# Kernel tuning notes

Measured on AMD Instinct MI355X. Metric: run time of the kernel, lower is better.

The kernel has to match this reference:

```python
import jax, jax.numpy as jnp
import numpy as np

H = 16
EMB = 1024
DH = 64  # att_dim


def setup_inputs() -> dict:
    key = jax.random.key(0)
    k1, k2, k3 = jax.random.split(key, 3)
    B, T = 4, 2048
    x = jax.random.normal(k1, (B, T, EMB), dtype=jnp.float32)
    # torch nn.Linear weight layout: [out_features, in_features]
    w_qkv = jax.random.normal(k2, (3 * H * DH, EMB), dtype=jnp.float32) * (1.0 / np.sqrt(EMB))
    wo = jax.random.normal(k3, (EMB, H * DH), dtype=jnp.float32) * (1.0 / np.sqrt(H * DH))
    return {"x": x, "w_qkv": w_qkv, "wo": wo}


def reference(x, w_qkv, wo):
    B, T, C = x.shape
    qkv = jnp.einsum('btc,oc->bto', x, w_qkv)  # [B,T,3*H*DH]
    q, k, v = jnp.split(qkv, 3, axis=-1)
    # [B,H,T,DH]
    q = q.reshape(B, T, H, DH).transpose(0, 2, 1, 3)
    k = k.reshape(B, T, H, DH).transpose(0, 2, 1, 3)
    v = v.reshape(B, T, H, DH).transpose(0, 2, 1, 3)
    scale = 1.0 / np.sqrt(DH).astype(np.float32)
    scores = jnp.einsum('bhqd,bhkd->bhqk', q, k) * scale
    causal = jnp.tril(jnp.ones((T, T), dtype=bool))
    scores = jnp.where(causal, scores, jnp.finfo(scores.dtype).min)
    attn = jax.nn.softmax(scores, axis=-1)
    y = jnp.einsum('bhqk,bhkd->bhqd', attn, v)  # [B,H,T,DH]
    y = y.transpose(0, 2, 1, 3).reshape(B, T, H * DH)
    return jnp.einsum('bti,oi->bto', y, wo)
```

## Files before the change

### kernel.cpp

```cpp
#include <hip/hip_runtime.h>
#include <hip/hip_bf16.h>
#include <stdint.h>


typedef __attribute__((ext_vector_type(8))) short short8;
typedef __attribute__((ext_vector_type(4))) float floatx4;

extern "C" __device__ float __ocml_native_exp2_f32(float);

__device__ __forceinline__ ushort f2bf(float f) {
  uint32_t u = __float_as_uint(f);
  u += 0x7fff + ((u >> 16) & 1);
  return (ushort)(u >> 16);
}

#if __has_builtin(__builtin_amdgcn_cvt_pk_bf16_f32)
typedef __attribute__((ext_vector_type(2))) __bf16 bf16x2;
__device__ __forceinline__ uint32_t pack_bf16(float a, float b) {
  union { bf16x2 v; uint32_t u; } cv;
  cv.v = __builtin_amdgcn_cvt_pk_bf16_f32(a, b);
  return cv.u;
}
#else
__device__ __forceinline__ uint32_t pack_bf16(float a, float b) {
  uint32_t ua = __float_as_uint(a) + 0x8000u;
  uint32_t ub = __float_as_uint(b) + 0x8000u;
  return __builtin_amdgcn_perm(ub, ua, 0x07060302u);
}
#endif

__device__ __forceinline__ void gload16(const ushort* g, ushort* l) {
  __builtin_amdgcn_global_load_lds(
      (const __attribute__((address_space(1))) void*)g,
      (__attribute__((address_space(3))) void*)l, 16, 0, 0);
}

__global__ __launch_bounds__(256) void cvt3_kernel(const float* __restrict__ x,
                                                   const float* __restrict__ wq,
                                                   const float* __restrict__ wo,
                                                   ushort* __restrict__ xo,
                                                   ushort* __restrict__ wqo,
                                                   ushort* __restrict__ woo) {
  int i = blockIdx.x * 256 + threadIdx.x;
  const float* in; ushort* out; int idx;
  if (i < 2097152)      { in = x;  out = xo;  idx = i; }
  else if (i < 2883584) { in = wq; out = wqo; idx = i - 2097152; }
  else                  { in = wo; out = woo; idx = i - 2883584; }
  float4 v = ((const float4*)in)[idx];
  ushort4 o;
  o.x = f2bf(v.x); o.y = f2bf(v.y); o.z = f2bf(v.z); o.w = f2bf(v.w);
  ((ushort4*)out)[idx] = o;
}

__global__ __launch_bounds__(512) void gemm256(const ushort* __restrict__ A,
                                               const ushort* __restrict__ Bw,
                                               ushort* __restrict__ qb,
                                               ushort* __restrict__ kb,
                                               ushort* __restrict__ vt) {
  constexpr int SLOT = 12288;
  __shared__ ushort ring[3 * SLOT];
  int tid = threadIdx.x;
  int lane = tid & 63, wave = tid >> 6;
  int lrow = lane & 15, quad = lane >> 4;
  int wm = wave >> 1, wn = wave & 1;
  int wm64 = wm * 64, wn64 = wn * 64;
  int m0 = blockIdx.x * 256, n0 = blockIdx.y * 128;

  int srow = tid >> 2;
  int schunk8 = ((tid & 3) ^ ((tid >> 3) & 3)) * 8;
  const ushort* Ag0 = A + (size_t)(m0 + srow) * 1024 + schunk8;
  const ushort* Ag1 = Ag0 + (size_t)128 * 1024;
  const ushort* Bg0 = Bw + (size_t)(n0 + srow) * 1024 + schunk8;
  int fo2 = (quad ^ ((lrow >> 1) & 3)) * 8;

  const floatx4 zero4 = {0.f, 0.f, 0.f, 0.f};
  floatx4 acc[4][4];
#pragma unroll
  for (int i = 0; i < 4; i++)
#pragma unroll
    for (int j = 0; j < 4; j++) acc[i][j] = zero4;

  auto stage = [&](int t) {
    ushort* Sa = &ring[(t % 3) * SLOT];
    size_t kk = (size_t)t * 32;
    gload16(Ag0 + kk, &Sa[wave * 16 * 32]);
    gload16(Ag1 + kk, &Sa[(128 + wave * 16) * 32]);
    gload16(Bg0 + kk, &Sa[8192 + wave * 16 * 32]);
  };

  short8 fAa[4], fAb[4], fBa[4], fBb[4];

#define READF(u_, FN)                                                         \
  {                                                                           \
    ushort* As_ = &ring[((u_) % 3) * SLOT];                                   \
    ushort* Bs_ = As_ + 8192;                                                 \
    _Pragma("unroll")                                                         \
    for (int mi = 0; mi < 4; mi++)                                            \
      FN##a[mi] = *(const short8*)(&As_[(wm64 + mi * 16 + lrow) * 32 + fo2]); \
    _Pragma("unroll")                                                         \
    for (int nj = 0; nj < 4; nj++)                                            \
      FN##b[nj] = *(const short8*)(&Bs_[(wn64 + nj * 16 + lrow) * 32 + fo2]); \
  }

#define MFMAS(FC)                                                             \
  {                                                                           \
    __builtin_amdgcn_s_setprio(1);                                            \
    _Pragma("unroll")                                                         \
    for (int mi = 0; mi < 4; mi++)                                            \
      _Pragma("unroll")                                                       \
      for (int nj = 0; nj < 4; nj++)                                          \
        acc[mi][nj] = __builtin_amdgcn_mfma_f32_16x16x32_bf16(                \
            FC##a[mi], FC##b[nj], acc[mi][nj], 0, 0, 0);                      \
    __builtin_amdgcn_s_setprio(0);                                            \
  }

#define BARRIER(N_)                                                           \
  asm volatile("s_waitcnt vmcnt(" #N_ ")" ::: "memory");                      \
  __builtin_amdgcn_s_barrier();                                               \
  asm volatile("" ::: "memory");

#define KITER(u_, N_, ISSUE_, FC, FN)                                         \
  {                                                                           \
    BARRIER(N_)                                                               \
    READF(u_, FN)                                                             \
    if (ISSUE_) stage((u_) + 2);                                              \
    MFMAS(FC)                                                                 \
  }

  stage(0); stage(1);
  BARRIER(3)
  READF(0, fA)
  stage(2);
#pragma unroll 1
  for (int p = 0; p < 14; ++p) {
    KITER(2 * p + 1, 3, true, fA, fB);
    KITER(2 * p + 2, 3, true, fB, fA);
  }
  KITER(29, 3, true, fA, fB);
  KITER(30, 3, false, fB, fA);
  KITER(31, 0, false, fA, fB);
  MFMAS(fB)

#undef KITER
#undef BARRIER
#undef MFMAS
#undef READF

  constexpr int CS = 136;
  ushort* sm = ring;
  int sec = n0 >> 10;
  int hrow = tid >> 4, kcol = tid & 15;
  __syncthreads();

  if (sec < 2) {
    float qs = (sec == 0) ? 0.18033688f : 1.0f;
    ushort* dst = (sec == 0) ? qb : kb;
    int hbase = n0 & 1023;
#pragma unroll 1
    for (int hf = 0; hf < 2; ++hf) {
      if ((wm >> 1) == hf) {
#pragma unroll
        for (int mi = 0; mi < 4; mi++)
#pragma unroll
          for (int nj = 0; nj < 4; nj++)
#pragma unroll
            for (int r = 0; r < 4; r++)
              sm[((wm & 1) * 64 + mi * 16 + quad * 4 + r) * CS +
                 wn64 + nj * 16 + lrow] = f2bf(acc[mi][nj][r] * qs);
      }
      __syncthreads();
#pragma unroll
      for (int mi = 0; mi < 4; mi++) {
        int mloc = mi * 32 + hrow;
        int m = m0 + hf * 128 + mloc, b_ = m >> 11, t = m & 2047;
        int col = kcol * 8;
        int h = (hbase + col) >> 6, d = col & 63;
        uint4 val = *(const uint4*)(&sm[mloc * CS + col]);
        *(uint4*)(dst + ((size_t)(b_ * 16 + h) * 2048 + t) * 64 + d) = val;
      }
      __syncthreads();
    }
  } else {
    int b_ = m0 >> 11, t0 = m0 & 2047;
#pragma unroll 1
    for (int hf = 0; hf < 2; ++hf) {
      if ((wm >> 1) == hf) {
#pragma unroll
        for (int mi = 0; mi < 4; mi++)
#pragma unroll
          for (int nj = 0; nj < 4; nj++) {
            uint2 w;
            w.x = pack_bf16(acc[mi][nj][0], acc[mi][nj][1]);
            w.y = pack_bf16(acc[mi][nj][2], acc[mi][nj][3]);
            *(uint2*)(&sm[(wn64 + nj * 16 + lrow) * CS +
                          (wm & 1) * 64 + mi * 16 + quad * 4]) = w;
          }
      }
      __syncthreads();
#pragma unroll
      for (int di = 0; di < 4; di++) {
        int nloc = di * 32 + hrow;
        int n = n0 + nloc, h = (n & 1023) >> 6, d = n & 63;
        uint4 val = *(const uint4*)(&sm[nloc * CS + kcol * 8]);
        *(uint4*)(vt + ((size_t)(b_ * 16 + h) * 64 + d) * 2048 +
                  t0 + hf * 128 + kcol * 8) = val;
      }
      __syncthreads();
    }
  }
}

__global__ __launch_bounds__(256) void gemm_out(const ushort* __restrict__ A,
                                                const ushort* __restrict__ Bw,
                                                float* __restrict__ Cf) {
  constexpr int SLOT = 8192;
  __shared__ ushort ring[3 * SLOT];
  int tid = threadIdx.x;
  int lane = tid & 63, wave = tid >> 6;
  int lrow = lane & 15, quad = lane >> 4;
  int wr = (wave >> 1) * 64, wc = (wave & 1) * 64;
  int m0 = blockIdx.x * 128, n0 = blockIdx.y * 128;

  int srow = tid >> 2;
  int schunk8 = ((tid & 3) ^ ((tid >> 3) & 3)) * 8;
  const ushort* Ag0 = A + (size_t)(m0 + srow) * 1024 + schunk8;
  const ushort* Ag1 = Ag0 + (size_t)64 * 1024;
  const ushort* Bg0 = Bw + (size_t)(n0 + srow) * 1024 + schunk8;
  const ushort* Bg1 = Bg0 + (size_t)64 * 1024;
  int fo2 = (quad ^ ((lrow >> 1) & 3)) * 8;

  const floatx4 zero4 = {0.f, 0.f, 0.f, 0.f};
  floatx4 acc[4][4];
#pragma unroll
  for (int i = 0; i < 4; i++)
#pragma unroll
    for (int j = 0; j < 4; j++) acc[i][j] = zero4;

  auto stage = [&](int t) {
    ushort* Sa = &ring[(t % 3) * SLOT];
    size_t kk = (size_t)t * 32;
    gload16(Ag0 + kk, &Sa[wave * 16 * 32]);
    gload16(Ag1 + kk, &Sa[(64 + wave * 16) * 32]);
    gload16(Bg0 + kk, &Sa[4096 + wave * 16 * 32]);
    gload16(Bg1 + kk, &Sa[4096 + (64 + wave * 16) * 32]);
  };

  short8 fAa[4], fAb[4], fBa[4], fBb[4];

#define READF(u_, FN)                                                         \
  {                                                                           \
    ushort* As_ = &ring[((u_) % 3) * SLOT];                                   \
    ushort* Bs_ = As_ + 4096;                                                 \
    _Pragma("unroll")                                                         \
    for (int mi = 0; mi < 4; mi++)                                            \
      FN##a[mi] = *(const short8*)(&As_[(wr + mi * 16 + lrow) * 32 + fo2]);   \
    _Pragma("unroll")                                                         \
    for (int nj = 0; nj < 4; nj++)                                            \
      FN##b[nj] = *(const short8*)(&Bs_[(wc + nj * 16 + lrow) * 32 + fo2]);   \
  }

#define MFMAS(FC)                                                             \
  {                                                                           \
    __builtin_amdgcn_s_setprio(1);                                            \
    _Pragma("unroll")                                                         \
    for (int mi = 0; mi < 4; mi++)                                            \
      _Pragma("unroll")                                                       \
      for (int nj = 0; nj < 4; nj++)                                          \
        acc[mi][nj] = __builtin_amdgcn_mfma_f32_16x16x32_bf16(                \
            FC##a[mi], FC##b[nj], acc[mi][nj], 0, 0, 0);                      \
    __builtin_amdgcn_s_setprio(0);                                            \
  }

#define BARRIER(N_)                                                           \
  asm volatile("s_waitcnt vmcnt(" #N_ ")" ::: "memory");                      \
  __builtin_amdgcn_s_barrier();                                               \
  asm volatile("" ::: "memory");

#define KITER(u_, N_, ISSUE_, FC, FN)                                         \
  {                                                                           \
    BARRIER(N_)                                                               \
    READF(u_, FN)                                                             \
    if (ISSUE_) stage((u_) + 2);                                              \
    MFMAS(FC)                                                                 \
  }

  stage(0); stage(1);
  BARRIER(4)
  READF(0, fA)
  stage(2);
#pragma unroll 1
  for (int p = 0; p < 14; ++p) {
    KITER(2 * p + 1, 4, true, fA, fB);
    KITER(2 * p + 2, 4, true, fB, fA);
  }
  KITER(29, 4, true, fA, fB);
  KITER(30, 4, false, fB, fA);
  KITER(31, 0, false, fA, fB);
  MFMAS(fB)

#undef KITER
#undef BARRIER
#undef MFMAS
#undef READF

#pragma unroll
  for (int mi = 0; mi < 4; mi++)
#pragma unroll
    for (int nj = 0; nj < 4; nj++)
#pragma unroll
      for (int r = 0; r < 4; r++) {
        int m = m0 + wr + mi * 16 + quad * 4 + r;
        int n = n0 + wc + nj * 16 + lrow;
        Cf[(size_t)m * 1024 + n] = acc[mi][nj][r];
      }
}

__global__ __launch_bounds__(512) void attn_kernel(const ushort* __restrict__ qg,
                                                   const ushort* __restrict__ kg,
                                                   const ushort* __restrict__ vg,
                                                   ushort* __restrict__ y) {
  __shared__ ushort Ks[64 * 64];
  __shared__ ushort Vs[64 * 64];
  __shared__ ushort Ps[8 * 16 * 72];
  int tid = threadIdx.x;
  int lane = tid & 63, wave = tid >> 6;
  int lrow = lane & 15, quad = lane >> 4;
  int gx = blockIdx.x, gy = blockIdx.y;
  int pr = gy >> 3;
  int bh = (gy & 7) * 8 + gx;
  const ushort* qp = qg + (size_t)bh * 2048 * 64;
  const ushort* kp = kg + (size_t)bh * 2048 * 64;
  const ushort* vp = vg + (size_t)bh * 64 * 2048;
  int b = bh >> 4, h = bh & 15;
  int srow = tid >> 3, sc = tid & 7;
  int sswz = ((sc ^ (srow & 7)) * 8);
  int fo = (quad ^ (lrow & 7)) * 8;
  ushort* Pw = &Ps[wave * 16 * 72];

  const floatx4 zero4 = {0.f, 0.f, 0.f, 0.f};
  short8 ones;
#pragma unroll
  for (int i = 0; i < 8; i++) ones[i] = (short)0x3F80;

#pragma unroll 1
  for (int pass = 0; pass < 2; ++pass) {
    int qt = pass ? (15 - pr) : pr;
    int last = 2 * qt + 1;

    const ushort* qrow_p = qp + (size_t)((qt << 7) + wave * 16 + lrow) * 64;
    short8 a_q0 = *(const short8*)(qrow_p + quad * 8);
    short8 a_q1 = *(const short8*)(qrow_p + (quad ^ 4) * 8);

    uint4 kreg = *(const uint4*)(kp + (size_t)srow * 64 + sc * 8);
    uint4 vreg = *(const uint4*)(vp + (size_t)srow * 2048 + sc * 8);

    floatx4 l_acc = zero4;
    floatx4 o_acc[4];
#pragma unroll
    for (int j = 0; j < 4; j++) o_acc[j] = zero4;

#pragma unroll 1
    for (int kv = 0; kv <= last; kv++) {
      asm volatile("" ::: "memory");
      __builtin_amdgcn_s_barrier();
      asm volatile("" ::: "memory");
      *(uint4*)(&Ks[srow * 64 + sswz]) = kreg;
      *(uint4*)(&Vs[srow * 64 + sswz]) = vreg;
      if (kv < last) {
        kreg = *(const uint4*)(kp + (size_t)((kv + 1) * 64 + srow) * 64 + sc * 8);
        vreg = *(const uint4*)(vp + (size_t)srow * 2048 + (kv + 1) * 64 + sc * 8);
      }
      asm volatile("s_waitcnt lgkmcnt(0)" ::: "memory");
      __builtin_amdgcn_s_barrier();
      asm volatile("" ::: "memory");

      floatx4 s[4];
#pragma unroll
      for (int ct = 0; ct < 4; ct++) {
        short8 k0 = *(const short8*)(&Ks[(ct * 16 + lrow) * 64 + fo]);
        short8 k1 = *(const short8*)(&Ks[(ct * 16 + lrow) * 64 + (fo ^ 32)]);
        floatx4 z = zero4;
        z = __builtin_amdgcn_mfma_f32_16x16x32_bf16(k0, a_q0, z, 0, 0, 0);
        z = __builtin_amdgcn_mfma_f32_16x16x32_bf16(k1, a_q1, z, 0, 0, 0);
        s[ct] = z;
      }

      if (kv >= 2 * qt) {
        int qabs = (qt << 7) + wave * 16 + lrow;
        int kbase = (kv << 6) + quad * 4;
#pragma unroll
        for (int ct = 0; ct < 4; ct++)
#pragma unroll
          for (int r = 0; r < 4; r++)
            if (kbase + ct * 16 + r > qabs) s[ct][r] = -1e30f;
      }

#pragma unroll
      for (int ct = 0; ct < 4; ct++) {
        float p0 = __ocml_native_exp2_f32(s[ct][0]);
        float p1 = __ocml_native_exp2_f32(s[ct][1]);
        float p2 = __ocml_native_exp2_f32(s[ct][2]);
        float p3 = __ocml_native_exp2_f32(s[ct][3]);
        uint2 w;
        w.x = pack_bf16(p0, p1);
        w.y = pack_bf16(p2, p3);
        *(uint2*)(&Pw[lrow * 72 + ct * 16 + quad * 4]) = w;
      }
      asm volatile("" ::: "memory");

      short8 a_p0 = *(const short8*)(&Pw[lrow * 72 + quad * 8]);
      short8 a_p1 = *(const short8*)(&Pw[lrow * 72 + 32 + quad * 8]);
      l_acc = __builtin_amdgcn_mfma_f32_16x16x32_bf16(a_p0, ones, l_acc, 0, 0, 0);
      l_acc = __builtin_amdgcn_mfma_f32_16x16x32_bf16(a_p1, ones, l_acc, 0, 0, 0);
#pragma unroll
      for (int j = 0; j < 4; j++) {
        short8 v0 = *(const short8*)(&Vs[(j * 16 + lrow) * 64 + fo]);
        short8 v1 = *(const short8*)(&Vs[(j * 16 + lrow) * 64 + (fo ^ 32)]);
        o_acc[j] = __builtin_amdgcn_mfma_f32_16x16x32_bf16(a_p0, v0, o_acc[j], 0, 0, 0);
        o_acc[j] = __builtin_amdgcn_mfma_f32_16x16x32_bf16(a_p1, v1, o_acc[j], 0, 0, 0);
      }
    }

    float inv[4];
#pragma unroll
    for (int r = 0; r < 4; r++) inv[r] = 1.0f / l_acc[r];

#pragma unroll
    for (int j = 0; j < 4; j++)
#pragma unroll
      for (int r = 0; r < 4; r++) {
        int t = (qt << 7) + wave * 16 + quad * 4 + r;
        y[((size_t)b * 2048 + t) * 1024 + h * 64 + j * 16 + lrow] =
            f2bf(o_acc[j][r] * inv[r]);
      }
  }
}

extern "C" void kernel_launch(void* const* d_in, const int* in_sizes, int n_in,
                              void* d_out, int out_size, void* d_ws, size_t ws_size,
                              hipStream_t stream) {
  const float* x     = (const float*)d_in[0];
  const float* w_qkv = (const float*)d_in[1];
  const float* wo    = (const float*)d_in[2];
  float* out = (float*)d_out;

  ushort* x_bf    = (ushort*)d_ws;
  ushort* wqkv_bf = x_bf + (size_t)8192 * 1024;
  ushort* wo_bf   = wqkv_bf + (size_t)3072 * 1024;
  ushort* qb      = wo_bf + (size_t)1024 * 1024;
  ushort* kb      = qb + (size_t)8388608;
  ushort* vt      = kb + (size_t)8388608;
  ushort* yb      = x_bf;

  cvt3_kernel<<<12288, 256, 0, stream>>>(x, w_qkv, wo, x_bf, wqkv_bf, wo_bf);
  gemm256<<<dim3(32, 24), 512, 0, stream>>>(x_bf, wqkv_bf, qb, kb, vt);
  attn_kernel<<<dim3(8, 64), 512, 0, stream>>>(qb, kb, vt, yb);
  gemm_out<<<dim3(64, 8), 256, 0, stream>>>(yb, wo_bf, out);
}
```

Measured before the change: 218.7 us.

## Enlarge QKV GEMM tile to 256x256 with 8-wide per-wave M fragments

Grows the QKV projection GEMM block tile from 256x128 to 256x256, with waves arranged 2x4 and each wave computing 128x64 (32 accumulators). The aim is more operand reuse per loaded byte and half as many blocks, 384 instead of 768. The register double-buffering of fragments is replaced by a single fragment load per iteration with rotating slot indices, and the epilogue is rewritten for the wider tile. The cost is higher register pressure and shared memory (96KB ring), lower occupancy, and a 384-block grid that may fill the CUs unevenly.

Result: slower. 227.0 us (+3.8%).

```diff
diff --git a/kernel.cpp b/kernel.cpp
--- a/kernel.cpp
+++ b/kernel.cpp
@@ -57,154 +57,148 @@
                                                ushort* __restrict__ qb,
                                                ushort* __restrict__ kb,
                                                ushort* __restrict__ vt) {
-  constexpr int SLOT = 12288;
+  constexpr int SLOT = 16384;
   __shared__ ushort ring[3 * SLOT];
   int tid = threadIdx.x;
   int lane = tid & 63, wave = tid >> 6;
   int lrow = lane & 15, quad = lane >> 4;
-  int wm = wave >> 1, wn = wave & 1;
-  int wm64 = wm * 64, wn64 = wn * 64;
-  int m0 = blockIdx.x * 256, n0 = blockIdx.y * 128;
+  int wm = wave >> 2, wn = wave & 3;
+  int wm128 = wm * 128, wn64 = wn * 64;
+  int m0 = blockIdx.x * 256, n0 = blockIdx.y * 256;
 
   int srow = tid >> 2;
   int schunk8 = ((tid & 3) ^ ((tid >> 3) & 3)) * 8;
   const ushort* Ag0 = A + (size_t)(m0 + srow) * 1024 + schunk8;
   const ushort* Ag1 = Ag0 + (size_t)128 * 1024;
   const ushort* Bg0 = Bw + (size_t)(n0 + srow) * 1024 + schunk8;
+  const ushort* Bg1 = Bg0 + (size_t)128 * 1024;
   int fo2 = (quad ^ ((lrow >> 1) & 3)) * 8;
 
   const floatx4 zero4 = {0.f, 0.f, 0.f, 0.f};
-  floatx4 acc[4][4];
-#pragma unroll
-  for (int i = 0; i < 4; i++)
+  floatx4 acc[8][4];
+#pragma unroll
+  for (int i = 0; i < 8; i++)
 #pragma unroll
     for (int j = 0; j < 4; j++) acc[i][j] = zero4;
 
-  auto stage = [&](int t) {
-    ushort* Sa = &ring[(t % 3) * SLOT];
+  auto stage = [&](int slot, int t) {
+    ushort* Sa = &ring[slot * SLOT];
     size_t kk = (size_t)t * 32;
-    gload16(Ag0 + kk, &Sa[wave * 16 * 32]);
-    gload16(Ag1 + kk, &Sa[(128 + wave * 16) * 32]);
-    gload16(Bg0 + kk, &Sa[8192 + wave * 16 * 32]);
+    gload16(Ag0 + kk, &Sa[wave * 512]);
+    gload16(Ag1 + kk, &Sa[4096 + wave * 512]);
+    gload16(Bg0 + kk, &Sa[8192 + wave * 512]);
+    gload16(Bg1 + kk, &Sa[12288 + wave * 512]);
   };
-
-  short8 fAa[4], fAb[4], fBa[4], fBb[4];
-
-#define READF(u_, FN)                                                         \
-  {                                                                           \
-    ushort* As_ = &ring[((u_) % 3) * SLOT];                                   \
-    ushort* Bs_ = As_ + 8192;                                                 \
-    _Pragma("unroll")                                                         \
-    for (int mi = 0; mi < 4; mi++)                                            \
-      FN##a[mi] = *(const short8*)(&As_[(wm64 + mi * 16 + lrow) * 32 + fo2]); \
-    _Pragma("unroll")                                                         \
-    for (int nj = 0; nj < 4; nj++)                                            \
-      FN##b[nj] = *(const short8*)(&Bs_[(wn64 + nj * 16 + lrow) * 32 + fo2]); \
-  }
-
-#define MFMAS(FC)                                                             \
-  {                                                                           \
-    __builtin_amdgcn_s_setprio(1);                                            \
-    _Pragma("unroll")                                                         \
-    for (int mi = 0; mi < 4; mi++)                                            \
-      _Pragma("unroll")                                                       \
-      for (int nj = 0; nj < 4; nj++)                                          \
-        acc[mi][nj] = __builtin_amdgcn_mfma_f32_16x16x32_bf16(                \
-            FC##a[mi], FC##b[nj], acc[mi][nj], 0, 0, 0);                      \
-    __builtin_amdgcn_s_setprio(0);                                            \
-  }
 
 #define BARRIER(N_)                                                           \
   asm volatile("s_waitcnt vmcnt(" #N_ ")" ::: "memory");                      \
   __builtin_amdgcn_s_barrier();                                               \
   asm volatile("" ::: "memory");
 
-#define KITER(u_, N_, ISSUE_, FC, FN)                                         \
+#define COMPUTE(CUR_, DOSTAGE_, NXT_, T_)                                     \
   {                                                                           \
-    BARRIER(N_)                                                               \
-    READF(u_, FN)                                                             \
-    if (ISSUE_) stage((u_) + 2);                                              \
-    MFMAS(FC)                                                                 \
-  }
-
-  stage(0); stage(1);
-  BARRIER(3)
-  READF(0, fA)
-  stage(2);
-#pragma unroll 1
-  for (int p = 0; p < 14; ++p) {
-    KITER(2 * p + 1, 3, true, fA, fB);
-    KITER(2 * p + 2, 3, true, fB, fA);
-  }
-  KITER(29, 3, true, fA, fB);
-  KITER(30, 3, false, fB, fA);
-  KITER(31, 0, false, fA, fB);
-  MFMAS(fB)
-
-#undef KITER
+    ushort* As_ = &ring[(CUR_)*SLOT];                                         \
+    ushort* Bs_ = As_ + 8192;                                                 \
+    short8 a_[8], b_[4];                                                      \
+    _Pragma("unroll")                                                         \
+    for (int mi = 0; mi < 8; mi++)                                            \
+      a_[mi] = *(const short8*)(&As_[(wm128 + mi * 16 + lrow) * 32 + fo2]);   \
+    _Pragma("unroll")                                                         \
+    for (int nj = 0; nj < 4; nj++)                                            \
+      b_[nj] = *(const short8*)(&Bs_[(wn64 + nj * 16 + lrow) * 32 + fo2]);    \
+    if (DOSTAGE_) stage((NXT_), (T_));                                        \
+    __builtin_amdgcn_s_setprio(1);                                            \
+    _Pragma("unroll")                                                         \
+    for (int mi = 0; mi < 8; mi++)                                            \
+      _Pragma("unroll")                                                       \
+      for (int nj = 0; nj < 4; nj++)                                          \
+        acc[mi][nj] = __builtin_amdgcn_mfma_f32_16x16x32_bf16(                \
+            a_[mi], b_[nj], acc[mi][nj], 0, 0, 0);                            \
+    __builtin_amdgcn_s_setprio(0);                                            \
+  }
+
+  stage(0, 0); stage(1, 1);
+  int cur = 0, nxt = 2;
+#pragma unroll 1
+  for (int u = 0; u < 30; ++u) {
+    BARRIER(4)
+    COMPUTE(cur, true, nxt, u + 2)
+    cur = (cur == 2) ? 0 : cur + 1;
+    nxt = (nxt == 2) ? 0 : nxt + 1;
+  }
+  BARRIER(4)
+  COMPUTE(cur, false, 0, 0)
+  cur = (cur == 2) ? 0 : cur + 1;
+  BARRIER(0)
+  COMPUTE(cur, false, 0, 0)
+
+#undef COMPUTE
 #undef BARRIER
-#undef MFMAS
-#undef READF
-
-  constexpr int CS = 136;
+
+  constexpr int CS = 264;
   ushort* sm = ring;
   int sec = n0 >> 10;
-  int hrow = tid >> 4, kcol = tid & 15;
+  int b_ = m0 >> 11, t0 = m0 & 2047;
+  int hb = (n0 & 1023) >> 6;
   __syncthreads();
 
   if (sec < 2) {
     float qs = (sec == 0) ? 0.18033688f : 1.0f;
     ushort* dst = (sec == 0) ? qb : kb;
-    int hbase = n0 & 1023;
+    int kcol = tid & 7, hrow = tid >> 3;
 #pragma unroll 1
     for (int hf = 0; hf < 2; ++hf) {
-      if ((wm >> 1) == hf) {
-#pragma unroll
-        for (int mi = 0; mi < 4; mi++)
+      if (wm == hf) {
+#pragma unroll
+        for (int mi = 0; mi < 8; mi++)
 #pragma unroll
           for (int nj = 0; nj < 4; nj++)
 #pragma unroll
             for (int r = 0; r < 4; r++)
-              sm[((wm & 1) * 64 + mi * 16 + quad * 4 + r) * CS +
-                 wn64 + nj * 16 + lrow] = f2bf(acc[mi][nj][r] * qs);
+              sm[(mi * 16 + quad * 4 + r) * CS + wn64 + nj * 16 + lrow] =
+                  f2bf(acc[mi][nj][r] * qs);
       }
       __syncthreads();
 #pragma unroll
-      for (int mi = 0; mi < 4; mi++) {
-        int mloc = mi * 32 + hrow;
-        int m = m0 + hf * 128 + mloc, b_ = m >> 11, t = m & 2047;
-        int col = kcol * 8;
-        int h = (hbase + col) >> 6, d = col & 63;
-        uint4 val = *(const uint4*)(&sm[mloc * CS + col]);
-        *(uint4*)(dst + ((size_t)(b_ * 16 + h) * 2048 + t) * 64 + d) = val;
-      }
+      for (int ri = 0; ri < 2; ri++)
+#pragma unroll
+        for (int hh = 0; hh < 4; hh++) {
+          int mloc = ri * 64 + hrow;
+          uint4 val = *(const uint4*)(&sm[mloc * CS + hh * 64 + kcol * 8]);
+          int t = t0 + hf * 128 + mloc;
+          *(uint4*)(dst + ((size_t)(b_ * 16 + hb + hh) * 2048 + t) * 64 +
+                    kcol * 8) = val;
+        }
       __syncthreads();
     }
   } else {
-    int b_ = m0 >> 11, t0 = m0 & 2047;
-#pragma unroll 1
-    for (int hf = 0; hf < 2; ++hf) {
-      if ((wm >> 1) == hf) {
-#pragma unroll
-        for (int mi = 0; mi < 4; mi++)
+    int kcol = tid & 15, drow = tid >> 4;
+#pragma unroll 1
+    for (int nf = 0; nf < 2; ++nf) {
+      if ((wn >> 1) == nf) {
+#pragma unroll
+        for (int mi = 0; mi < 8; mi++)
 #pragma unroll
           for (int nj = 0; nj < 4; nj++) {
             uint2 w;
             w.x = pack_bf16(acc[mi][nj][0], acc[mi][nj][1]);
             w.y = pack_bf16(acc[mi][nj][2], acc[mi][nj][3]);
-            *(uint2*)(&sm[(wn64 + nj * 16 + lrow) * CS +
-                          (wm & 1) * 64 + mi * 16 + quad * 4]) = w;
+            *(uint2*)(&sm[((wn & 1) * 64 + nj * 16 + lrow) * CS + wm128 +
+                          mi * 16 + quad * 4]) = w;
           }
       }
       __syncthreads();
 #pragma unroll
-      for (int di = 0; di < 4; di++) {
-        int nloc = di * 32 + hrow;
-        int n = n0 + nloc, h = (n & 1023) >> 6, d = n & 63;
-        uint4 val = *(const uint4*)(&sm[nloc * CS + kcol * 8]);
-        *(uint4*)(vt + ((size_t)(b_ * 16 + h) * 64 + d) * 2048 +
-                  t0 + hf * 128 + kcol * 8) = val;
-      }
+      for (int di = 0; di < 4; di++)
+#pragma unroll
+        for (int mi2 = 0; mi2 < 2; mi2++) {
+          int nloc = di * 32 + drow;
+          int moff = mi2 * 128 + kcol * 8;
+          uint4 val = *(const uint4*)(&sm[nloc * CS + moff]);
+          int h = hb + nf * 2 + (nloc >> 6), d = nloc & 63;
+          *(uint4*)(vt + ((size_t)(b_ * 16 + h) * 64 + d) * 2048 + t0 +
+                    moff) = val;
+        }
       __syncthreads();
     }
   }
@@ -453,7 +447,7 @@
   ushort* yb      = x_bf;
 
   cvt3_kernel<<<12288, 256, 0, stream>>>(x, w_qkv, wo, x_bf, wqkv_bf, wo_bf);
-  gemm256<<<dim3(32, 24), 512, 0, stream>>>(x_bf, wqkv_bf, qb, kb, vt);
+  gemm256<<<dim3(32, 12), 512, 0, stream>>>(x_bf, wqkv_bf, qb, kb, vt);
   attn_kernel<<<dim3(8, 64), 512, 0, stream>>>(qb, kb, vt, yb);
   gemm_out<<<dim3(64, 8), 256, 0, stream>>>(yb, wo_bf, out);
 }
```
